# Kernel optimization log

Hardware: AMD Instinct MI355X
Metric: run time of the kernel (lower is better)

The kernel has to match this reference:

```python
import jax, jax.numpy as jnp
import numpy as np

NUM_ITERATIONS = 3


def squash(x, axis):
    # squared_norm/(1+squared_norm) * x / sqrt(squared_norm), as in the torch module
    sn = jnp.sum(x * x, axis=axis, keepdims=True)
    return sn / (1.0 + sn) * x / jnp.sqrt(sn)


def setup_inputs() -> dict:
    key = jax.random.key(0)
    k1, k2 = jax.random.split(key)
    batch, num_caps, num_route, in_ch, out_ch = 32, 32, 4608, 8, 16
    x = jax.random.normal(k1, (batch, num_route, in_ch), dtype=jnp.float32)
    route_weights = jax.random.normal(k2, (num_caps, num_route, in_ch, out_ch), dtype=jnp.float32)
    return {"x": x, "route_weights": route_weights}


def reference(x, route_weights):
    # U[b,c,r,1,o] = x[b,1,r,1,i] @ W[1,c,r,i,o]
    U = jnp.einsum("bri,crio->bcro", x, route_weights)[:, :, :, None, :]  # [b,c,r,1,o]
    B = jnp.zeros_like(U)
    V = None
    for _ in range(NUM_ITERATIONS):
        C = jax.nn.softmax(B, axis=1)                 # softmax over capsules
        S = jnp.sum(C * U, axis=2, keepdims=True)      # reduce over route nodes: [b,c,1,1,o]
        V = squash(S, axis=-1)
        B = B + U * V
    b, c = B.shape[0], B.shape[1]
    o = B.shape[-1]
    return V.reshape(b, c, o)
```

## Files before the change

### kernel.cpp

```cpp
#include <hip/hip_runtime.h>

#define BATCH 32
#define NCAPS 32
#define NR    4608
#define NI    8
#define NO    16
#define CSTR  200
#define MAXRB 36
#define NCH   256
#define L2E   1.44269504088896341f

typedef float f2 __attribute__((ext_vector_type(2)));

template<int RB, bool FIRST>
__global__ __launch_bounds__(1024, 2) void caps_route_fast(
    const float* __restrict__ x,
    const float* __restrict__ W,
    const float* __restrict__ A,
    float* __restrict__ P)
{
    constexpr int NP = RB / 2;
    __shared__ __align__(16) float Ws[2][2][NCAPS * CSTR];
    __shared__ __align__(16) f2    xP[RB][8][2][NI];

    const int t  = threadIdx.x;
    const int om = (t & 3) | (((t >> 3) & 1) << 2);
    const int co = ((t >> 4) & 1) | (((t >> 2) & 1) << 1) | (((t >> 5) & 1) << 2);
    const int w  = t >> 6;
    const int oh = w & 1;
    const int bq = w >> 1;
    const int o  = oh * 8 + om;
    const int b0 = 4 * bq;
    const int r0 = blockIdx.x * RB;

    f2 a2[2][4];
    if (!FIRST) {
#pragma unroll
        for (int p = 0; p < 2; ++p)
#pragma unroll
            for (int cl = 0; cl < 4; ++cl) {
                const int c = 4 * co + cl;
                a2[p][cl].x = A[((b0 + 2 * p + 0) * NCAPS + c) * NO + o] * L2E;
                a2[p][cl].y = A[((b0 + 2 * p + 1) * NCAPS + c) * NO + o] * L2E;
            }
    }
    f2 acc[2][4];
#pragma unroll
    for (int p = 0; p < 2; ++p)
#pragma unroll
        for (int cl = 0; cl < 4; ++cl) acc[p][cl] = (f2)0.f;

    for (int s = t; s < RB * 16; s += 1024) {
        const int rr = s >> 4, bp = s & 15;
        const float* xp0 = &x[((size_t)(2 * bp + 0) * NR + r0 + rr) * NI];
        const float* xp1 = &x[((size_t)(2 * bp + 1) * NR + r0 + rr) * NI];
        const float4 a0 = *(const float4*)xp0;
        const float4 a1 = *(const float4*)(xp0 + 4);
        const float4 c0 = *(const float4*)xp1;
        const float4 c1 = *(const float4*)(xp1 + 4);
        f2* d = &xP[rr][bp >> 1][bp & 1][0];
        d[0] = f2{a0.x, c0.x}; d[1] = f2{a0.y, c0.y};
        d[2] = f2{a0.z, c0.z}; d[3] = f2{a0.w, c0.w};
        d[4] = f2{a1.x, c1.x}; d[5] = f2{a1.y, c1.y};
        d[6] = f2{a1.z, c1.z}; d[7] = f2{a1.w, c1.w};
    }

    const int c_st = t >> 5;
    const int sl   = (c_st >> 2) + 8 * (c_st & 3);
    const int part = t & 31;
    const int i_st = part >> 2;
    const int o0   = (part & 3) * 4;
    const int dst  = sl * CSTR + o0 * 12 + i_st;
    const float* wsrc = W + ((size_t)c_st * NR + r0) * (NI * NO) + part * 4;

    {
        const float4 s0 = *(const float4*)wsrc;
        const float4 s1 = *(const float4*)(wsrc + NI * NO);
        float* d0 = &Ws[0][0][dst];
        d0[0] = s0.x; d0[12] = s0.y; d0[24] = s0.z; d0[36] = s0.w;
        float* d1 = &Ws[0][1][dst];
        d1[0] = s1.x; d1[12] = s1.y; d1[24] = s1.z; d1[36] = s1.w;
    }
    float4 pfa = {}, pfb = {};
    if (NP > 1) {
        pfa = *(const float4*)(wsrc + 2 * NI * NO);
        pfb = *(const float4*)(wsrc + 3 * NI * NO);
    }
    __syncthreads();

    auto compute_r = [&](const float* wt, const f2* xv) {
        f2 xq[2][NI];
#pragma unroll
        for (int i = 0; i < NI; ++i) { xq[0][i] = xv[i]; xq[1][i] = xv[NI + i]; }
        const float* wb = wt + co * CSTR + o * 12;
        if (FIRST) {
#pragma unroll
            for (int cl = 0; cl < 4; ++cl) {
                const float* wp = wb + cl * (8 * CSTR);
                const float4 w0 = *(const float4*)wp;
                const float4 w1 = *(const float4*)(wp + 4);
#pragma unroll
                for (int p = 0; p < 2; ++p) {
                    f2 u2 = xq[p][0] * w0.x;
                    u2 += xq[p][1] * w0.y;
                    u2 += xq[p][2] * w0.z;
                    u2 += xq[p][3] * w0.w;
                    u2 += xq[p][4] * w1.x;
                    u2 += xq[p][5] * w1.y;
                    u2 += xq[p][6] * w1.z;
                    u2 += xq[p][7] * w1.w;
                    acc[p][cl] += u2;
                }
            }
        } else {
            f2 tt[2][4];
            f2 Z0 = (f2)0.f, Z1 = (f2)0.f;
#pragma unroll
            for (int cl = 0; cl < 4; ++cl) {
                const float* wp = wb + cl * (8 * CSTR);
                const float4 w0 = *(const float4*)wp;
                const float4 w1 = *(const float4*)(wp + 4);
                f2 u0 = xq[0][0] * w0.x;
                u0 += xq[0][1] * w0.y;
                u0 += xq[0][2] * w0.z;
                u0 += xq[0][3] * w0.w;
                u0 += xq[0][4] * w1.x;
                u0 += xq[0][5] * w1.y;
                u0 += xq[0][6] * w1.z;
                u0 += xq[0][7] * w1.w;
                f2 u1 = xq[1][0] * w0.x;
                u1 += xq[1][1] * w0.y;
                u1 += xq[1][2] * w0.z;
                u1 += xq[1][3] * w0.w;
                u1 += xq[1][4] * w1.x;
                u1 += xq[1][5] * w1.y;
                u1 += xq[1][6] * w1.z;
                u1 += xq[1][7] * w1.w;
                const f2 l0 = u0 * a2[0][cl];
                const f2 l1 = u1 * a2[1][cl];
                f2 e0, e1;
                e0.x = exp2f(l0.x); e0.y = exp2f(l0.y);
                e1.x = exp2f(l1.x); e1.y = exp2f(l1.y);
                Z0 += e0; Z1 += e1;
                tt[0][cl] = e0 * u0;
                tt[1][cl] = e1 * u1;
            }
#pragma unroll
            for (int m = 0; m < 3; ++m) {
                const int msk = (m == 0) ? 4 : (m == 1) ? 16 : 32;
                Z0.x += __shfl_xor(Z0.x, msk); Z0.y += __shfl_xor(Z0.y, msk);
                Z1.x += __shfl_xor(Z1.x, msk); Z1.y += __shfl_xor(Z1.y, msk);
            }
            f2 rz0, rz1;
            rz0.x = __builtin_amdgcn_rcpf(Z0.x); rz0.y = __builtin_amdgcn_rcpf(Z0.y);
            rz1.x = __builtin_amdgcn_rcpf(Z1.x); rz1.y = __builtin_amdgcn_rcpf(Z1.y);
#pragma unroll
            for (int cl = 0; cl < 4; ++cl) {
                acc[0][cl] += tt[0][cl] * rz0;
                acc[1][cl] += tt[1][cl] * rz1;
            }
        }
    };

#pragma unroll 1
    for (int rp = 0; rp < NP; ++rp) {
        const int cur = rp & 1;

        if (rp + 1 < NP) {
            float* d0 = &Ws[cur ^ 1][0][dst];
            d0[0] = pfa.x; d0[12] = pfa.y; d0[24] = pfa.z; d0[36] = pfa.w;
            float* d1 = &Ws[cur ^ 1][1][dst];
            d1[0] = pfb.x; d1[12] = pfb.y; d1[24] = pfb.z; d1[36] = pfb.w;
            if (rp + 2 < NP) {
                pfa = *(const float4*)(wsrc + (size_t)(2 * rp + 4) * (NI * NO));
                pfb = *(const float4*)(wsrc + (size_t)(2 * rp + 5) * (NI * NO));
            }
        }

        compute_r(&Ws[cur][0][0], &xP[2 * rp + 0][bq][0][0]);
        compute_r(&Ws[cur][1][0], &xP[2 * rp + 1][bq][0][0]);
        __syncthreads();
    }

#pragma unroll
    for (int bb = 0; bb < 4; ++bb) {
        const int p = bb >> 1, h = bb & 1;
        float* pout = P + (((size_t)blockIdx.x * BATCH + b0 + bb) * NO + o) * NCAPS + 4 * co;
        float4 v;
        v.x = h ? acc[p][0].y : acc[p][0].x;
        v.y = h ? acc[p][1].y : acc[p][1].x;
        v.z = h ? acc[p][2].y : acc[p][2].x;
        v.w = h ? acc[p][3].y : acc[p][3].x;
        if (FIRST) { v.x *= 0.03125f; v.y *= 0.03125f; v.z *= 0.03125f; v.w *= 0.03125f; }
        *(float4*)pout = v;
    }
}

__global__ __launch_bounds__(256) void caps_partial(const float* __restrict__ P,
                                                    float* __restrict__ P2)
{
    const int tid = threadIdx.x;
    const int ct  = blockIdx.x & 15;
    const int rg  = blockIdx.x >> 4;
    const size_t col = (size_t)ct * 1024 + tid * 4;
    const float* p = P + (size_t)rg * 16 * 16384 + col;
    float4 s = {0.f, 0.f, 0.f, 0.f};
#pragma unroll
    for (int k = 0; k < 16; ++k) {
        const float4 v = *(const float4*)(p + (size_t)k * 16384);
        s.x += v.x; s.y += v.y; s.z += v.z; s.w += v.w;
    }
    *(float4*)(P2 + (size_t)rg * 16384 + col) = s;
}

__global__ void caps_reduce_squash(const float* __restrict__ P,
                                   float* __restrict__ A,
                                   float* __restrict__ out,
                                   int nchunk)
{
    __shared__ float sm[256];
    const int bc  = blockIdx.x;
    const int b   = bc >> 5;
    const int c   = bc & 31;
    const int tid = threadIdx.x;
    const int o = tid & 15;
    const int j = tid >> 4;
    float s = 0.f;
    for (int tch = j; tch < nchunk; tch += 16)
        s += P[(((size_t)tch * BATCH + b) * NO + o) * NCAPS + c];
    sm[tid] = s;
    __syncthreads();
    if (tid < 16) {
        float S = 0.f;
#pragma unroll
        for (int k = 0; k < 16; ++k) S += sm[tid + 16 * k];
        float sq = S * S;
#pragma unroll
        for (int d = 8; d >= 1; d >>= 1) sq += __shfl_xor(sq, d, 16);
        const float scale = sq / ((1.f + sq) * sqrtf(sq));
        const float V = S * scale;
        const int idx = bc * NO + tid;
        A[idx] += V;
        if (out) out[idx] = V;
    }
}

__global__ __launch_bounds__(512, 2) void caps_route_generic(
    const float* __restrict__ x, const float* __restrict__ W,
    const float* __restrict__ A, float* __restrict__ P, int rb)
{
    __shared__ __align__(16) float Ws[NCAPS * CSTR];
    __shared__ __align__(16) float xsT[NI * MAXRB * BATCH];

    const int t = threadIdx.x;
    const int b = t & 31;
    const int o = t >> 5;
    const int r0 = blockIdx.x * rb;
    const int rbs = rb * BATCH;

    float a2s[NCAPS];
#pragma unroll
    for (int c = 0; c < NCAPS; ++c)
        a2s[c] = A[(b * NCAPS + c) * NO + o] * L2E;
    float acc[NCAPS];
#pragma unroll
    for (int c = 0; c < NCAPS; ++c) acc[c] = 0.f;

    for (int s = t; s < rbs; s += 512) {
        const int rr = s >> 5, bb = s & 31;
        const float4 v0 = *(const float4*)&x[((size_t)bb * NR + r0 + rr) * NI];
        const float4 v1 = *(const float4*)&x[((size_t)bb * NR + r0 + rr) * NI + 4];
        const float tmp[8] = {v0.x, v0.y, v0.z, v0.w, v1.x, v1.y, v1.z, v1.w};
#pragma unroll
        for (int i = 0; i < NI; ++i) xsT[i * rbs + s] = tmp[i];
    }

    const int cs  = t >> 4;
    const int seg = t & 15;
    const int iw  = seg >> 1;
    const int ob  = (seg & 1) * 8;
    const float* wsrc = W + ((size_t)cs * NR + r0) * (NI * NO) + seg * 8;
    float4 pf0 = *(const float4*)wsrc;
    float4 pf1 = *(const float4*)(wsrc + 4);

    for (int rr = 0; rr < rb; ++rr) {
        __syncthreads();
        {
            const float tmp[8] = {pf0.x, pf0.y, pf0.z, pf0.w,
                                  pf1.x, pf1.y, pf1.z, pf1.w};
#pragma unroll
            for (int k = 0; k < 8; ++k)
                Ws[cs * CSTR + (ob + k) * 12 + iw] = tmp[k];
        }
        if (rr + 1 < rb) {
            wsrc += NI * NO;
            pf0 = *(const float4*)wsrc;
            pf1 = *(const float4*)(wsrc + 4);
        }
        __syncthreads();

        float xq[NI];
#pragma unroll
        for (int i = 0; i < NI; ++i) xq[i] = xsT[i * rbs + rr * 32 + b];

        float tt[NCAPS];
        float Z = 0.f;
        const float* bp = &Ws[o * 12];
#pragma unroll
        for (int c = 0; c < NCAPS; ++c) {
            const float* wp = bp + c * CSTR;
            const float4 w0 = *(const float4*)wp;
            const float4 w1 = *(const float4*)(wp + 4);
            float uu =      xq[0] * w0.x;
            uu = fmaf(xq[1], w0.y, uu);
            uu = fmaf(xq[2], w0.z, uu);
            uu = fmaf(xq[3], w0.w, uu);
            uu = fmaf(xq[4], w1.x, uu);
            uu = fmaf(xq[5], w1.y, uu);
            uu = fmaf(xq[6], w1.z, uu);
            uu = fmaf(xq[7], w1.w, uu);
            const float ee = exp2f(uu * a2s[c]);
            Z += ee;
            tt[c] = ee * uu;
        }
        const float rz = __builtin_amdgcn_rcpf(Z);
#pragma unroll
        for (int c = 0; c < NCAPS; ++c)
            acc[c] = fmaf(tt[c], rz, acc[c]);
    }

    float* pout = P + (((size_t)blockIdx.x * BATCH + b) * NO + o) * NCAPS;
#pragma unroll
    for (int q = 0; q < NCAPS / 4; ++q) {
        float4 v;
        v.x = acc[4 * q + 0]; v.y = acc[4 * q + 1];
        v.z = acc[4 * q + 2]; v.w = acc[4 * q + 3];
        *(float4*)(pout + 4 * q) = v;
    }
}

__global__ void caps_zero(float* __restrict__ p, int n)
{
    const int i = blockIdx.x * blockDim.x + threadIdx.x;
    if (i < n) p[i] = 0.f;
}

extern "C" void kernel_launch(void* const* d_in, const int* in_sizes, int n_in,
                              void* d_out, int out_size, void* d_ws, size_t ws_size,
                              hipStream_t stream)
{
    const float* x = (const float*)d_in[0];
    const float* W = (const float*)d_in[1];
    float* out = (float*)d_out;

    float* A  = (float*)d_ws;
    float* P  = A + BATCH * NCAPS * NO;
    float* P2 = P + (size_t)NCH * BATCH * NCAPS * NO;

    const size_t elem = (size_t)BATCH * NCAPS * NO;
    caps_zero<<<(int)((elem + 255) / 256), 256, 0, stream>>>(A, (int)elem);

    if ((size_t)(1 + NCH + 16) * elem * sizeof(float) <= ws_size) {
        caps_route_fast<NR / NCH, true><<<NCH, 1024, 0, stream>>>(x, W, A, P);
        caps_partial<<<256, 256, 0, stream>>>(P, P2);
        caps_reduce_squash<<<BATCH * NCAPS, 256, 0, stream>>>(P2, A, nullptr, 16);
        caps_route_fast<NR / NCH, false><<<NCH, 1024, 0, stream>>>(x, W, A, P);
        caps_partial<<<256, 256, 0, stream>>>(P, P2);
        caps_reduce_squash<<<BATCH * NCAPS, 256, 0, stream>>>(P2, A, nullptr, 16);
        caps_route_fast<NR / NCH, false><<<NCH, 1024, 0, stream>>>(x, W, A, P);
        caps_partial<<<256, 256, 0, stream>>>(P, P2);
        caps_reduce_squash<<<BATCH * NCAPS, 256, 0, stream>>>(P2, A, out, 16);
    } else {
        int nchunk = 128;
        while (nchunk > 32 &&
               (size_t)(nchunk + 1) * elem * sizeof(float) > ws_size)
            nchunk >>= 1;
        const int rb = NR / nchunk;
        for (int it = 0; it < 3; ++it) {
            caps_route_generic<<<nchunk, 512, 0, stream>>>(x, W, A, P, rb);
            caps_reduce_squash<<<BATCH * NCAPS, 256, 0, stream>>>(
                P, A, it == 2 ? out : nullptr, nchunk);
        }
    }
}
```

Before: 150.6 us.

## Store W in native layout in LDS and remap threads to output pairs

The fast routing kernel now copies W tiles into shared memory with float4 stores in their natural [i][o] order (stride 136) instead of a transposed scatter with stride 200. Each thread now computes two adjacent outputs for two batches using f2 loads along o. The partial-sum layout P changes from [chunk,b,o,c] to [chunk,b,c,o], and the reduce and generic kernels are updated to match. The aim is to cut scalar LDS stores and bank conflicts during staging and to give coalesced writes. In exchange the softmax shuffle pattern changes and LDS reads become 8-byte rather than 16-byte.

Measured after the change: 183.7 us. +22.0%, slower.

```diff
diff --git a/kernel.cpp b/kernel.cpp
--- a/kernel.cpp
+++ b/kernel.cpp
@@ -5,6 +5,7 @@
 #define NR    4608
 #define NI    8
 #define NO    16
+#define CSTRW 136
 #define CSTR  200
 #define MAXRB 36
 #define NCH   256
@@ -20,144 +21,118 @@
     float* __restrict__ P)
 {
     constexpr int NP = RB / 2;
-    __shared__ __align__(16) float Ws[2][2][NCAPS * CSTR];
+    __shared__ __align__(16) float Ws[2][2][NCAPS * CSTRW];
     __shared__ __align__(16) f2    xP[RB][8][2][NI];
 
-    const int t  = threadIdx.x;
-    const int om = (t & 3) | (((t >> 3) & 1) << 2);
-    const int co = ((t >> 4) & 1) | (((t >> 2) & 1) << 1) | (((t >> 5) & 1) << 2);
-    const int w  = t >> 6;
-    const int oh = w & 1;
-    const int bq = w >> 1;
-    const int o  = oh * 8 + om;
-    const int b0 = 4 * bq;
-    const int r0 = blockIdx.x * RB;
+    const int t   = threadIdx.x;
+    const int op2 = t & 7;
+    const int co  = (t >> 3) & 7;
+    const int bp  = t >> 6;
+    const int b0  = 2 * bp;
+    const int o0  = 2 * op2;
+    const int chunk = blockIdx.x;
+    const int r0  = chunk * RB;
 
     f2 a2[2][4];
     if (!FIRST) {
 #pragma unroll
-        for (int p = 0; p < 2; ++p)
-#pragma unroll
-            for (int cl = 0; cl < 4; ++cl) {
-                const int c = 4 * co + cl;
-                a2[p][cl].x = A[((b0 + 2 * p + 0) * NCAPS + c) * NO + o] * L2E;
-                a2[p][cl].y = A[((b0 + 2 * p + 1) * NCAPS + c) * NO + o] * L2E;
-            }
+        for (int bb = 0; bb < 2; ++bb)
+#pragma unroll
+            for (int cl = 0; cl < 4; ++cl)
+                a2[bb][cl] = *(const f2*)&A[((b0 + bb) * NCAPS + 4 * co + cl) * NO + o0]
+                             * L2E;
     }
     f2 acc[2][4];
 #pragma unroll
-    for (int p = 0; p < 2; ++p)
-#pragma unroll
-        for (int cl = 0; cl < 4; ++cl) acc[p][cl] = (f2)0.f;
+    for (int bb = 0; bb < 2; ++bb)
+#pragma unroll
+        for (int cl = 0; cl < 4; ++cl) acc[bb][cl] = (f2)0.f;
 
     for (int s = t; s < RB * 16; s += 1024) {
-        const int rr = s >> 4, bp = s & 15;
-        const float* xp0 = &x[((size_t)(2 * bp + 0) * NR + r0 + rr) * NI];
-        const float* xp1 = &x[((size_t)(2 * bp + 1) * NR + r0 + rr) * NI];
+        const int rr = s >> 4, pq = s & 15;
+        const float* xp0 = &x[((size_t)(2 * pq + 0) * NR + r0 + rr) * NI];
+        const float* xp1 = &x[((size_t)(2 * pq + 1) * NR + r0 + rr) * NI];
         const float4 a0 = *(const float4*)xp0;
         const float4 a1 = *(const float4*)(xp0 + 4);
         const float4 c0 = *(const float4*)xp1;
         const float4 c1 = *(const float4*)(xp1 + 4);
-        f2* d = &xP[rr][bp >> 1][bp & 1][0];
+        f2* d = &xP[rr][pq >> 1][pq & 1][0];
         d[0] = f2{a0.x, c0.x}; d[1] = f2{a0.y, c0.y};
         d[2] = f2{a0.z, c0.z}; d[3] = f2{a0.w, c0.w};
         d[4] = f2{a1.x, c1.x}; d[5] = f2{a1.y, c1.y};
         d[6] = f2{a1.z, c1.z}; d[7] = f2{a1.w, c1.w};
     }
 
-    const int c_st = t >> 5;
-    const int sl   = (c_st >> 2) + 8 * (c_st & 3);
-    const int part = t & 31;
-    const int i_st = part >> 2;
-    const int o0   = (part & 3) * 4;
-    const int dst  = sl * CSTR + o0 * 12 + i_st;
-    const float* wsrc = W + ((size_t)c_st * NR + r0) * (NI * NO) + part * 4;
+    const int c_st  = t >> 5;
+    const int sl_st = (c_st >> 2) + 8 * (c_st & 3);
+    const int part  = t & 31;
+    const int sub_r = part >> 4;
+    const int q     = part & 15;
+    const int dstf  = sl_st * CSTRW + q * 4;
+    const float* wsrc = W + ((size_t)c_st * NR + r0 + sub_r) * (NI * NO) + q * 4;
 
     {
         const float4 s0 = *(const float4*)wsrc;
-        const float4 s1 = *(const float4*)(wsrc + NI * NO);
-        float* d0 = &Ws[0][0][dst];
-        d0[0] = s0.x; d0[12] = s0.y; d0[24] = s0.z; d0[36] = s0.w;
-        float* d1 = &Ws[0][1][dst];
-        d1[0] = s1.x; d1[12] = s1.y; d1[24] = s1.z; d1[36] = s1.w;
-    }
-    float4 pfa = {}, pfb = {};
+        const float4 s1 = *(const float4*)(wsrc + 64);
+        *(float4*)&Ws[0][sub_r][dstf]      = s0;
+        *(float4*)&Ws[0][sub_r][dstf + 64] = s1;
+    }
+    float4 pf0 = {}, pf1 = {};
     if (NP > 1) {
-        pfa = *(const float4*)(wsrc + 2 * NI * NO);
-        pfb = *(const float4*)(wsrc + 3 * NI * NO);
+        pf0 = *(const float4*)(wsrc + 256);
+        pf1 = *(const float4*)(wsrc + 256 + 64);
     }
     __syncthreads();
 
     auto compute_r = [&](const float* wt, const f2* xv) {
-        f2 xq[2][NI];
-#pragma unroll
-        for (int i = 0; i < NI; ++i) { xq[0][i] = xv[i]; xq[1][i] = xv[NI + i]; }
-        const float* wb = wt + co * CSTR + o * 12;
+        float xa[NI], xb[NI];
+#pragma unroll
+        for (int i = 0; i < NI; ++i) { xa[i] = xv[i].x; xb[i] = xv[i].y; }
+        f2 u[2][4];
+#pragma unroll
+        for (int cl = 0; cl < 4; ++cl) {
+            const float* wp = wt + (co + 8 * cl) * CSTRW + o0;
+            f2 u0 = (f2)0.f, u1 = (f2)0.f;
+#pragma unroll
+            for (int i = 0; i < NI; ++i) {
+                const f2 wv = *(const f2*)(wp + i * 16);
+                u0 += wv * xa[i];
+                u1 += wv * xb[i];
+            }
+            u[0][cl] = u0; u[1][cl] = u1;
+        }
         if (FIRST) {
 #pragma unroll
             for (int cl = 0; cl < 4; ++cl) {
-                const float* wp = wb + cl * (8 * CSTR);
-                const float4 w0 = *(const float4*)wp;
-                const float4 w1 = *(const float4*)(wp + 4);
-#pragma unroll
-                for (int p = 0; p < 2; ++p) {
-                    f2 u2 = xq[p][0] * w0.x;
-                    u2 += xq[p][1] * w0.y;
-                    u2 += xq[p][2] * w0.z;
-                    u2 += xq[p][3] * w0.w;
-                    u2 += xq[p][4] * w1.x;
-                    u2 += xq[p][5] * w1.y;
-                    u2 += xq[p][6] * w1.z;
-                    u2 += xq[p][7] * w1.w;
-                    acc[p][cl] += u2;
-                }
+                acc[0][cl] += u[0][cl];
+                acc[1][cl] += u[1][cl];
             }
         } else {
-            f2 tt[2][4];
             f2 Z0 = (f2)0.f, Z1 = (f2)0.f;
 #pragma unroll
             for (int cl = 0; cl < 4; ++cl) {
-                const float* wp = wb + cl * (8 * CSTR);
-                const float4 w0 = *(const float4*)wp;
-                const float4 w1 = *(const float4*)(wp + 4);
-                f2 u0 = xq[0][0] * w0.x;
-                u0 += xq[0][1] * w0.y;
-                u0 += xq[0][2] * w0.z;
-                u0 += xq[0][3] * w0.w;
-                u0 += xq[0][4] * w1.x;
-                u0 += xq[0][5] * w1.y;
-                u0 += xq[0][6] * w1.z;
-                u0 += xq[0][7] * w1.w;
-                f2 u1 = xq[1][0] * w0.x;
-                u1 += xq[1][1] * w0.y;
-                u1 += xq[1][2] * w0.z;
-                u1 += xq[1][3] * w0.w;
-                u1 += xq[1][4] * w1.x;
-                u1 += xq[1][5] * w1.y;
-                u1 += xq[1][6] * w1.z;
-                u1 += xq[1][7] * w1.w;
-                const f2 l0 = u0 * a2[0][cl];
-                const f2 l1 = u1 * a2[1][cl];
+                const f2 l0 = u[0][cl] * a2[0][cl];
+                const f2 l1 = u[1][cl] * a2[1][cl];
                 f2 e0, e1;
                 e0.x = exp2f(l0.x); e0.y = exp2f(l0.y);
                 e1.x = exp2f(l1.x); e1.y = exp2f(l1.y);
                 Z0 += e0; Z1 += e1;
-                tt[0][cl] = e0 * u0;
-                tt[1][cl] = e1 * u1;
-            }
-#pragma unroll
-            for (int m = 0; m < 3; ++m) {
-                const int msk = (m == 0) ? 4 : (m == 1) ? 16 : 32;
-                Z0.x += __shfl_xor(Z0.x, msk); Z0.y += __shfl_xor(Z0.y, msk);
-                Z1.x += __shfl_xor(Z1.x, msk); Z1.y += __shfl_xor(Z1.y, msk);
-            }
+                u[0][cl] *= e0;
+                u[1][cl] *= e1;
+            }
+            Z0.x += __shfl_xor(Z0.x, 8);  Z0.y += __shfl_xor(Z0.y, 8);
+            Z1.x += __shfl_xor(Z1.x, 8);  Z1.y += __shfl_xor(Z1.y, 8);
+            Z0.x += __shfl_xor(Z0.x, 16); Z0.y += __shfl_xor(Z0.y, 16);
+            Z1.x += __shfl_xor(Z1.x, 16); Z1.y += __shfl_xor(Z1.y, 16);
+            Z0.x += __shfl_xor(Z0.x, 32); Z0.y += __shfl_xor(Z0.y, 32);
+            Z1.x += __shfl_xor(Z1.x, 32); Z1.y += __shfl_xor(Z1.y, 32);
             f2 rz0, rz1;
             rz0.x = __builtin_amdgcn_rcpf(Z0.x); rz0.y = __builtin_amdgcn_rcpf(Z0.y);
             rz1.x = __builtin_amdgcn_rcpf(Z1.x); rz1.y = __builtin_amdgcn_rcpf(Z1.y);
 #pragma unroll
             for (int cl = 0; cl < 4; ++cl) {
-                acc[0][cl] += tt[0][cl] * rz0;
-                acc[1][cl] += tt[1][cl] * rz1;
+                acc[0][cl] += u[0][cl] * rz0;
+                acc[1][cl] += u[1][cl] * rz1;
             }
         }
     };
@@ -165,35 +140,27 @@
 #pragma unroll 1
     for (int rp = 0; rp < NP; ++rp) {
         const int cur = rp & 1;
-
         if (rp + 1 < NP) {
-            float* d0 = &Ws[cur ^ 1][0][dst];
-            d0[0] = pfa.x; d0[12] = pfa.y; d0[24] = pfa.z; d0[36] = pfa.w;
-            float* d1 = &Ws[cur ^ 1][1][dst];
-            d1[0] = pfb.x; d1[12] = pfb.y; d1[24] = pfb.z; d1[36] = pfb.w;
+            *(float4*)&Ws[cur ^ 1][sub_r][dstf]      = pf0;
+            *(float4*)&Ws[cur ^ 1][sub_r][dstf + 64] = pf1;
             if (rp + 2 < NP) {
-                pfa = *(const float4*)(wsrc + (size_t)(2 * rp + 4) * (NI * NO));
-                pfb = *(const float4*)(wsrc + (size_t)(2 * rp + 5) * (NI * NO));
-            }
-        }
-
-        compute_r(&Ws[cur][0][0], &xP[2 * rp + 0][bq][0][0]);
-        compute_r(&Ws[cur][1][0], &xP[2 * rp + 1][bq][0][0]);
+                pf0 = *(const float4*)(wsrc + (size_t)(rp + 2) * 256);
+                pf1 = *(const float4*)(wsrc + (size_t)(rp + 2) * 256 + 64);
+            }
+        }
+        compute_r(&Ws[cur][0][0], &xP[2 * rp + 0][bp >> 1][bp & 1][0]);
+        compute_r(&Ws[cur][1][0], &xP[2 * rp + 1][bp >> 1][bp & 1][0]);
         __syncthreads();
     }
 
 #pragma unroll
-    for (int bb = 0; bb < 4; ++bb) {
-        const int p = bb >> 1, h = bb & 1;
-        float* pout = P + (((size_t)blockIdx.x * BATCH + b0 + bb) * NO + o) * NCAPS + 4 * co;
-        float4 v;
-        v.x = h ? acc[p][0].y : acc[p][0].x;
-        v.y = h ? acc[p][1].y : acc[p][1].x;
-        v.z = h ? acc[p][2].y : acc[p][2].x;
-        v.w = h ? acc[p][3].y : acc[p][3].x;
-        if (FIRST) { v.x *= 0.03125f; v.y *= 0.03125f; v.z *= 0.03125f; v.w *= 0.03125f; }
-        *(float4*)pout = v;
-    }
+    for (int bb = 0; bb < 2; ++bb)
+#pragma unroll
+        for (int cl = 0; cl < 4; ++cl) {
+            f2 v = acc[bb][cl];
+            if (FIRST) v *= 0.03125f;
+            *(f2*)&P[(((size_t)chunk * BATCH + b0 + bb) * NCAPS + 4 * co + cl) * NO + o0] = v;
+        }
 }
 
 __global__ __launch_bounds__(256) void caps_partial(const float* __restrict__ P,
@@ -220,14 +187,12 @@
 {
     __shared__ float sm[256];
     const int bc  = blockIdx.x;
-    const int b   = bc >> 5;
-    const int c   = bc & 31;
     const int tid = threadIdx.x;
     const int o = tid & 15;
     const int j = tid >> 4;
     float s = 0.f;
     for (int tch = j; tch < nchunk; tch += 16)
-        s += P[(((size_t)tch * BATCH + b) * NO + o) * NCAPS + c];
+        s += P[((size_t)tch * (BATCH * NCAPS) + bc) * NO + o];
     sm[tid] = s;
     __syncthreads();
     if (tid < 16) {
@@ -305,10 +270,10 @@
 
         float tt[NCAPS];
         float Z = 0.f;
-        const float* bp = &Ws[o * 12];
+        const float* bp2 = &Ws[o * 12];
 #pragma unroll
         for (int c = 0; c < NCAPS; ++c) {
-            const float* wp = bp + c * CSTR;
+            const float* wp = bp2 + c * CSTR;
             const float4 w0 = *(const float4*)wp;
             const float4 w1 = *(const float4*)(wp + 4);
             float uu =      xq[0] * w0.x;
@@ -329,14 +294,9 @@
             acc[c] = fmaf(tt[c], rz, acc[c]);
     }
 
-    float* pout = P + (((size_t)blockIdx.x * BATCH + b) * NO + o) * NCAPS;
-#pragma unroll
-    for (int q = 0; q < NCAPS / 4; ++q) {
-        float4 v;
-        v.x = acc[4 * q + 0]; v.y = acc[4 * q + 1];
-        v.z = acc[4 * q + 2]; v.w = acc[4 * q + 3];
-        *(float4*)(pout + 4 * q) = v;
-    }
+    float* pout = P + (((size_t)blockIdx.x * BATCH + b) * NCAPS) * NO + o;
+#pragma unroll
+    for (int c = 0; c < NCAPS; ++c) pout[c * NO] = acc[c];
 }
 
 __global__ void caps_zero(float* __restrict__ p, int n)
```

## Cache prediction vectors in fp16 and reuse them across routing iterations

Applied to the files above, without the earlier changes.

Adds a first-iteration kernel that computes U = x·W, writes it to workspace as fp16, and accumulates the first-iteration partial sums. The later routing iterations run a lighter kernel that reads cached U instead of recomputing the matvec from x and W. This trades repeated FMA work and W loads for a large extra memory write and two reads of about 150 MB. It also adds fp16 rounding error to U, and it only activates when the workspace is large enough.

Measured after the change: 139.8 us. 1.08x faster.

```diff
diff --git a/kernel.cpp b/kernel.cpp
--- a/kernel.cpp
+++ b/kernel.cpp
@@ -11,13 +11,206 @@
 #define L2E   1.44269504088896341f
 
 typedef float f2 __attribute__((ext_vector_type(2)));
+typedef _Float16 half4v __attribute__((ext_vector_type(4)));
+typedef _Float16 half8v __attribute__((ext_vector_type(8)));
+
+template<int RB>
+__global__ __launch_bounds__(1024, 2) void caps_route_store(
+    const float* __restrict__ x,
+    const float* __restrict__ W,
+    float* __restrict__ P,
+    unsigned short* __restrict__ Uh)
+{
+    constexpr int NP = RB / 2;
+    __shared__ __align__(16) float Ws[2][2][NCAPS * CSTR];
+    __shared__ __align__(16) f2    xP[RB][8][2][NI];
+
+    const int t  = threadIdx.x;
+    const int om = (t & 3) | (((t >> 3) & 1) << 2);
+    const int co = ((t >> 4) & 1) | (((t >> 2) & 1) << 1) | (((t >> 5) & 1) << 2);
+    const int w  = t >> 6;
+    const int oh = w & 1;
+    const int bq = w >> 1;
+    const int o  = oh * 8 + om;
+    const int b0 = 4 * bq;
+    const int r0 = blockIdx.x * RB;
+
+    f2 acc[2][4];
+#pragma unroll
+    for (int p = 0; p < 2; ++p)
+#pragma unroll
+        for (int cl = 0; cl < 4; ++cl) acc[p][cl] = (f2)0.f;
+
+    for (int s = t; s < RB * 16; s += 1024) {
+        const int rr = s >> 4, bp = s & 15;
+        const float* xp0 = &x[((size_t)(2 * bp + 0) * NR + r0 + rr) * NI];
+        const float* xp1 = &x[((size_t)(2 * bp + 1) * NR + r0 + rr) * NI];
+        const float4 a0 = *(const float4*)xp0;
+        const float4 a1 = *(const float4*)(xp0 + 4);
+        const float4 c0 = *(const float4*)xp1;
+        const float4 c1 = *(const float4*)(xp1 + 4);
+        f2* d = &xP[rr][bp >> 1][bp & 1][0];
+        d[0] = f2{a0.x, c0.x}; d[1] = f2{a0.y, c0.y};
+        d[2] = f2{a0.z, c0.z}; d[3] = f2{a0.w, c0.w};
+        d[4] = f2{a1.x, c1.x}; d[5] = f2{a1.y, c1.y};
+        d[6] = f2{a1.z, c1.z}; d[7] = f2{a1.w, c1.w};
+    }
+
+    const int c_st = t >> 5;
+    const int sl   = (c_st >> 2) + 8 * (c_st & 3);
+    const int part = t & 31;
+    const int i_st = part >> 2;
+    const int o0   = (part & 3) * 4;
+    const int dst  = sl * CSTR + o0 * 12 + i_st;
+    const float* wsrc = W + ((size_t)c_st * NR + r0) * (NI * NO) + part * 4;
+
+    {
+        const float4 s0 = *(const float4*)wsrc;
+        const float4 s1 = *(const float4*)(wsrc + NI * NO);
+        float* d0 = &Ws[0][0][dst];
+        d0[0] = s0.x; d0[12] = s0.y; d0[24] = s0.z; d0[36] = s0.w;
+        float* d1 = &Ws[0][1][dst];
+        d1[0] = s1.x; d1[12] = s1.y; d1[24] = s1.z; d1[36] = s1.w;
+    }
+    float4 pfa = {}, pfb = {};
+    if (NP > 1) {
+        pfa = *(const float4*)(wsrc + 2 * NI * NO);
+        pfb = *(const float4*)(wsrc + 3 * NI * NO);
+    }
+    __syncthreads();
+
+    auto compute_store = [&](const float* wt, const f2* xv, int r) {
+        f2 xq[2][NI];
+#pragma unroll
+        for (int i = 0; i < NI; ++i) { xq[0][i] = xv[i]; xq[1][i] = xv[NI + i]; }
+        const float* wb = wt + co * CSTR + o * 12;
+        f2 u[2][4];
+#pragma unroll
+        for (int cl = 0; cl < 4; ++cl) {
+            const float* wp = wb + cl * (8 * CSTR);
+            const float4 w0 = *(const float4*)wp;
+            const float4 w1 = *(const float4*)(wp + 4);
+#pragma unroll
+            for (int p = 0; p < 2; ++p) {
+                f2 u2 = xq[p][0] * w0.x;
+                u2 += xq[p][1] * w0.y;
+                u2 += xq[p][2] * w0.z;
+                u2 += xq[p][3] * w0.w;
+                u2 += xq[p][4] * w1.x;
+                u2 += xq[p][5] * w1.y;
+                u2 += xq[p][6] * w1.z;
+                u2 += xq[p][7] * w1.w;
+                u[p][cl] = u2;
+                acc[p][cl] += u2;
+            }
+        }
+        unsigned short* ub = Uh + (((size_t)r * BATCH + b0) * NO + o) * NCAPS + 4 * co;
+#pragma unroll
+        for (int bb = 0; bb < 4; ++bb) {
+            const int p = bb >> 1, h = bb & 1;
+            half4v hv;
+            hv[0] = (_Float16)(h ? u[p][0].y : u[p][0].x);
+            hv[1] = (_Float16)(h ? u[p][1].y : u[p][1].x);
+            hv[2] = (_Float16)(h ? u[p][2].y : u[p][2].x);
+            hv[3] = (_Float16)(h ? u[p][3].y : u[p][3].x);
+            *(half4v*)(ub + (size_t)bb * (NO * NCAPS)) = hv;
+        }
+    };
+
+#pragma unroll 1
+    for (int rp = 0; rp < NP; ++rp) {
+        const int cur = rp & 1;
+        if (rp + 1 < NP) {
+            float* d0 = &Ws[cur ^ 1][0][dst];
+            d0[0] = pfa.x; d0[12] = pfa.y; d0[24] = pfa.z; d0[36] = pfa.w;
+            float* d1 = &Ws[cur ^ 1][1][dst];
+            d1[0] = pfb.x; d1[12] = pfb.y; d1[24] = pfb.z; d1[36] = pfb.w;
+            if (rp + 2 < NP) {
+                pfa = *(const float4*)(wsrc + (size_t)(2 * rp + 4) * (NI * NO));
+                pfb = *(const float4*)(wsrc + (size_t)(2 * rp + 5) * (NI * NO));
+            }
+        }
+        compute_store(&Ws[cur][0][0], &xP[2 * rp + 0][bq][0][0], r0 + 2 * rp + 0);
+        compute_store(&Ws[cur][1][0], &xP[2 * rp + 1][bq][0][0], r0 + 2 * rp + 1);
+        __syncthreads();
+    }
+
+#pragma unroll
+    for (int bb = 0; bb < 4; ++bb) {
+        const int p = bb >> 1, h = bb & 1;
+        float* pout = P + (((size_t)blockIdx.x * BATCH + b0 + bb) * NO + o) * NCAPS + 4 * co;
+        float4 v;
+        v.x = (h ? acc[p][0].y : acc[p][0].x) * 0.03125f;
+        v.y = (h ? acc[p][1].y : acc[p][1].x) * 0.03125f;
+        v.z = (h ? acc[p][2].y : acc[p][2].x) * 0.03125f;
+        v.w = (h ? acc[p][3].y : acc[p][3].x) * 0.03125f;
+        *(float4*)pout = v;
+    }
+}
+
+template<int RB>
+__global__ __launch_bounds__(1024, 2) void caps_route_cached(
+    const unsigned short* __restrict__ Uh,
+    const float* __restrict__ A,
+    float* __restrict__ P)
+{
+    const int t  = threadIdx.x;
+    const int ch = t & 1;
+    const int o  = (t >> 1) & 15;
+    const int b  = t >> 5;
+    const int r0 = blockIdx.x * RB;
+
+    float a2[16];
+#pragma unroll
+    for (int cc = 0; cc < 16; ++cc)
+        a2[cc] = A[(b * NCAPS + 16 * ch + cc) * NO + o] * L2E;
+    float acc[16];
+#pragma unroll
+    for (int cc = 0; cc < 16; ++cc) acc[cc] = 0.f;
+
+    const unsigned short* up =
+        Uh + (((size_t)r0 * BATCH + b) * NO + o) * NCAPS + ch * 16;
+
+#pragma unroll 1
+    for (int rr = 0; rr < RB; ++rr) {
+        const uint4 q0 = *(const uint4*)(up);
+        const uint4 q1 = *(const uint4*)(up + 8);
+        up += BATCH * NO * NCAPS;
+        const half8v h0 = __builtin_bit_cast(half8v, q0);
+        const half8v h1 = __builtin_bit_cast(half8v, q1);
+        float u[16];
+#pragma unroll
+        for (int k = 0; k < 8; ++k) { u[k] = (float)h0[k]; u[8 + k] = (float)h1[k]; }
+        float Z = 0.f;
+        float tt[16];
+#pragma unroll
+        for (int cc = 0; cc < 16; ++cc) {
+            const float uu = u[cc];
+            const float ee = exp2f(uu * a2[cc]);
+            Z += ee;
+            tt[cc] = ee * uu;
+        }
+        Z += __shfl_xor(Z, 1);
+        const float rz = __builtin_amdgcn_rcpf(Z);
+#pragma unroll
+        for (int cc = 0; cc < 16; ++cc)
+            acc[cc] = fmaf(tt[cc], rz, acc[cc]);
+    }
+
+    float* pout = P + (((size_t)blockIdx.x * BATCH + b) * NO + o) * NCAPS + ch * 16;
+#pragma unroll
+    for (int q = 0; q < 4; ++q) {
+        float4 v;
+        v.x = acc[4 * q + 0]; v.y = acc[4 * q + 1];
+        v.z = acc[4 * q + 2]; v.w = acc[4 * q + 3];
+        *(float4*)(pout + 4 * q) = v;
+    }
+}
 
 template<int RB, bool FIRST>
 __global__ __launch_bounds__(1024, 2) void caps_route_fast(
-    const float* __restrict__ x,
-    const float* __restrict__ W,
-    const float* __restrict__ A,
-    float* __restrict__ P)
+    const float* __restrict__ x, const float* __restrict__ W,
+    const float* __restrict__ A, float* __restrict__ P)
 {
     constexpr int NP = RB / 2;
     __shared__ __align__(16) float Ws[2][2][NCAPS * CSTR];
@@ -165,7 +358,6 @@
 #pragma unroll 1
     for (int rp = 0; rp < NP; ++rp) {
         const int cur = rp & 1;
-
         if (rp + 1 < NP) {
             float* d0 = &Ws[cur ^ 1][0][dst];
             d0[0] = pfa.x; d0[12] = pfa.y; d0[24] = pfa.z; d0[36] = pfa.w;
@@ -176,7 +368,6 @@
                 pfb = *(const float4*)(wsrc + (size_t)(2 * rp + 5) * (NI * NO));
             }
         }
-
         compute_r(&Ws[cur][0][0], &xP[2 * rp + 0][bq][0][0]);
         compute_r(&Ws[cur][1][0], &xP[2 * rp + 1][bq][0][0]);
         __syncthreads();
@@ -305,10 +496,10 @@
 
         float tt[NCAPS];
         float Z = 0.f;
-        const float* bp = &Ws[o * 12];
+        const float* bp2 = &Ws[o * 12];
 #pragma unroll
         for (int c = 0; c < NCAPS; ++c) {
-            const float* wp = bp + c * CSTR;
+            const float* wp = bp2 + c * CSTR;
             const float4 w0 = *(const float4*)wp;
             const float4 w1 = *(const float4*)(wp + 4);
             float uu =      xq[0] * w0.x;
@@ -353,14 +544,28 @@
     const float* W = (const float*)d_in[1];
     float* out = (float*)d_out;
 
+    const size_t elem = (size_t)BATCH * NCAPS * NO;
     float* A  = (float*)d_ws;
-    float* P  = A + BATCH * NCAPS * NO;
-    float* P2 = P + (size_t)NCH * BATCH * NCAPS * NO;
-
-    const size_t elem = (size_t)BATCH * NCAPS * NO;
+    float* P  = A + elem;
+    float* P2 = P + (size_t)NCH * elem;
+    unsigned short* Uh = (unsigned short*)(P2 + 16 * elem);
+
+    const size_t need_base = (size_t)(1 + NCH + 16) * elem * sizeof(float);
+    const size_t need_u    = (size_t)NR * elem * sizeof(unsigned short);
+
     caps_zero<<<(int)((elem + 255) / 256), 256, 0, stream>>>(A, (int)elem);
 
-    if ((size_t)(1 + NCH + 16) * elem * sizeof(float) <= ws_size) {
+    if (ws_size >= need_base + need_u) {
+        caps_route_store<NR / NCH><<<NCH, 1024, 0, stream>>>(x, W, P, Uh);
+        caps_partial<<<256, 256, 0, stream>>>(P, P2);
+        caps_reduce_squash<<<BATCH * NCAPS, 256, 0, stream>>>(P2, A, nullptr, 16);
+        caps_route_cached<NR / NCH><<<NCH, 1024, 0, stream>>>(Uh, A, P);
+        caps_partial<<<256, 256, 0, stream>>>(P, P2);
+        caps_reduce_squash<<<BATCH * NCAPS, 256, 0, stream>>>(P2, A, nullptr, 16);
+        caps_route_cached<NR / NCH><<<NCH, 1024, 0, stream>>>(Uh, A, P);
+        caps_partial<<<256, 256, 0, stream>>>(P, P2);
+        caps_reduce_squash<<<BATCH * NCAPS, 256, 0, stream>>>(P2, A, out, 16);
+    } else if (ws_size >= need_base) {
         caps_route_fast<NR / NCH, true><<<NCH, 1024, 0, stream>>>(x, W, A, P);
         caps_partial<<<256, 256, 0, stream>>>(P, P2);
         caps_reduce_squash<<<BATCH * NCAPS, 256, 0, stream>>>(P2, A, nullptr, 16);
```
